# Performance work log

Hardware: AMD Instinct MI355X
Metric: run time of the kernel (lower is better)

Reference implementation:

```python
import jax, jax.numpy as jnp
import numpy as np

B, C, T, V = 8, 64, 16, 207
H, WSZ = 8, 4
EPS = 1e-5


def setup_inputs() -> dict:
    key = jax.random.key(0)
    ks = jax.random.split(key, 16)
    def w(k, shape):
        return jax.random.normal(k, shape, jnp.float32) * 0.02
    inp = {"x": jax.random.normal(ks[0], (B, C, T, V), jnp.float32)}
    for i, s in enumerate("ab"):
        o = 1 + i * 4
        inp[f"qkv_w_{s}"] = w(ks[o], (C, 3 * C))
        inp[f"qkv_b_{s}"] = jnp.zeros((3 * C,), jnp.float32)
        inp[f"proj_w_{s}"] = w(ks[o + 1], (C, C))
        inp[f"proj_b_{s}"] = jnp.zeros((C,), jnp.float32)
        inp[f"ffn_w1_{s}"] = w(ks[o + 2], (C, 4 * C))
        inp[f"ffn_b1_{s}"] = jnp.zeros((4 * C,), jnp.float32)
        inp[f"ffn_w2_{s}"] = w(ks[o + 3], (4 * C, C))
        inp[f"ffn_b2_{s}"] = jnp.zeros((C,), jnp.float32)
        inp[f"ln_{s}1_g"] = jnp.ones((C, T, V), jnp.float32)
        inp[f"ln_{s}1_b"] = jnp.zeros((C, T, V), jnp.float32)
        inp[f"ln_{s}2_g"] = jnp.ones((C, T, V), jnp.float32)
        inp[f"ln_{s}2_b"] = jnp.zeros((C, T, V), jnp.float32)
    inp["n_head"] = H
    inp["window_size"] = WSZ
    return inp


def _layer_norm(x, g, b):
    # LayerNorm over (C, T, V) dims of [B, C, T, V]
    mu = jnp.mean(x, axis=(1, 2, 3), keepdims=True)
    var = jnp.var(x, axis=(1, 2, 3), keepdims=True)
    return (x - mu) / jnp.sqrt(var + EPS) * g + b


def _window_att(x, wqkv, bqkv, wo, bo, n_head, wsz):
    # Joint spatio-temporal attention within windows of `wsz` timesteps.
    b_, c_, t_, v_ = x.shape
    nw = t_ // wsz
    dh = c_ // n_head
    # [B,C,T,V] -> [B,T,V,C] -> [B,nW, wsz*V, C]
    xt = jnp.transpose(x, (0, 2, 3, 1)).reshape(b_, nw, wsz * v_, c_)
    qkv = xt @ wqkv + bqkv  # [B,nW,N,3C]
    q, k, v = jnp.split(qkv, 3, axis=-1)
    def heads(t):
        return t.reshape(b_, nw, -1, n_head, dh).transpose(0, 1, 3, 2, 4)  # [B,nW,H,N,dh]
    q, k, v = heads(q), heads(k), heads(v)
    scale = 1.0 / jnp.sqrt(jnp.asarray(dh, jnp.float32))
    att = jax.nn.softmax(jnp.einsum('bwhnd,bwhmd->bwhnm', q, k) * scale, axis=-1)
    out = jnp.einsum('bwhnm,bwhmd->bwhnd', att, v)
    out = out.transpose(0, 1, 3, 2, 4).reshape(b_, nw, wsz * v_, c_) @ wo + bo
    return out.reshape(b_, t_, v_, c_).transpose(0, 3, 1, 2)


def _ffn(x, w1, b1, w2, b2):
    h = jax.nn.relu(jnp.einsum('bctv,cd->bdtv', x, w1) + b1[None, :, None, None])
    return jnp.einsum('bdtv,dc->bctv', h, w2) + b2[None, :, None, None]


def _block(x, wqkv, bqkv, wo, bo, w1, b1, w2, b2, g1, be1, g2, be2, n_head, wsz):
    x = _window_att(x, wqkv, bqkv, wo, bo, n_head, wsz) + x
    x = _layer_norm(x, g1, be1)
    x = _ffn(x, w1, b1, w2, b2) + x
    x = _layer_norm(x, g2, be2)
    # cyclic shift along time by shift_pixel = wsz // 2
    return jnp.roll(x, -(wsz // 2), axis=2)


def reference(x, qkv_w_a, qkv_b_a, proj_w_a, proj_b_a, ffn_w1_a, ffn_b1_a, ffn_w2_a, ffn_b2_a,
              ln_a1_g, ln_a1_b, ln_a2_g, ln_a2_b,
              qkv_w_b, qkv_b_b, proj_w_b, proj_b_b, ffn_w1_b, ffn_b1_b, ffn_w2_b, ffn_b2_b,
              ln_b1_g, ln_b1_b, ln_b2_g, ln_b2_b, n_head, window_size):
    x = _block(x, qkv_w_a, qkv_b_a, proj_w_a, proj_b_a, ffn_w1_a, ffn_b1_a, ffn_w2_a, ffn_b2_a,
               ln_a1_g, ln_a1_b, ln_a2_g, ln_a2_b, n_head, window_size)
    x = _block(x, qkv_w_b, qkv_b_b, proj_w_b, proj_b_b, ffn_w1_b, ffn_b1_b, ffn_w2_b, ffn_b2_b,
               ln_b1_g, ln_b1_b, ln_b2_g, ln_b2_b, n_head, window_size)
    return x
```

## Files before the change

### kernel.cpp

```cpp
#include <hip/hip_runtime.h>
#include <hip/hip_bf16.h>

#define Bb  8
#define Cc  64
#define Tt  16
#define Vv  207
#define Hh  8
#define DH  8
#define NW  4
#define WSZ 4
#define Nn  (WSZ*Vv)
#define NP  832
#define TV  (Tt*Vv)
#define CTV (Cc*Tt*Vv)
#define S   (Bb*CTV)
#define NBWH (Bb*NW*Hh)
#define EPSF 1e-5f
#define QSCALE 0.51006971401146f

typedef __attribute__((ext_vector_type(4))) short bf16x4;
typedef __attribute__((ext_vector_type(4))) float f32x4;
typedef __attribute__((ext_vector_type(2))) unsigned int u32x2;

static __device__ __forceinline__ short f2bf(float f) {
    union { float f; unsigned u; } v; v.f = f;
    unsigned r = (v.u + 0x7FFFu + ((v.u >> 16) & 1u)) >> 16;
    return (short)r;
}

static __device__ __forceinline__ bf16x4 pack4(float a, float b, float c, float d) {
    unsigned ua = __builtin_bit_cast(unsigned, a) + 0x8000u;
    unsigned ub = __builtin_bit_cast(unsigned, b) + 0x8000u;
    unsigned uc = __builtin_bit_cast(unsigned, c) + 0x8000u;
    unsigned ud = __builtin_bit_cast(unsigned, d) + 0x8000u;
    u32x2 t;
    t[0] = (ua >> 16) | (ub & 0xFFFF0000u);
    t[1] = (uc >> 16) | (ud & 0xFFFF0000u);
    return __builtin_bit_cast(bf16x4, t);
}

__global__ void prep_kernel(short* __restrict__ qb, short* __restrict__ kb,
                            short* __restrict__ vtb, float* __restrict__ stats) {
    int i = blockIdx.x*256 + threadIdx.x;
    if (i < 64) stats[i] = 0.f;
    if (i < NBWH*NP*8) {
        int bwh = i / (NP*8); int rest = i % (NP*8);
        int n = rest >> 3; int d = 8 + (rest & 7);
        kb[((size_t)bwh*NP + n)*16 + d] = 0;
        int d2 = 8 + rest / NP; int n2 = rest % NP;
        vtb[((size_t)bwh*16 + d2)*NP + n2] = (d2 == 8) ? (short)0x3F80 : (short)0;
    }
    if (i < NBWH*32) {
        int bwh = i >> 5; int rest = i & 31;
        int n = Nn + (rest >> 3); int d = rest & 7;
        qb[((size_t)bwh*NP + n)*8 + d] = 0;
        kb[((size_t)bwh*NP + n)*16 + d] = 0;
        int d3 = rest >> 2; int n3 = Nn + (rest & 3);
        vtb[((size_t)bwh*16 + d3)*NP + n3] = 0;
    }
}

__global__ __launch_bounds__(256) void qkv_kernel(const float* __restrict__ src,
        const float* __restrict__ st, const float* __restrict__ g, const float* __restrict__ be,
        const float* __restrict__ w, const float* __restrict__ bias,
        short* __restrict__ qb, short* __restrict__ kb, short* __restrict__ vtb) {
    __shared__ short wqs[3072*4];
    __shared__ float bqs[192];
    __shared__ short os[64*196];
    int tid = threadIdx.x;
    int b = blockIdx.x / 52;
    int r0 = (blockIdx.x % 52) * 64;
    const float* xb = src + (size_t)b*CTV;
    for (int s = tid; s < 3072; s += 256) {
        int nt = s >> 8; int kc = (s >> 6) & 3; int ln = s & 63;
        int li = ln & 15; int q = ln >> 4;
        bf16x4 f;
        #pragma unroll
        for (int j = 0; j < 4; ++j)
            f[j] = f2bf(w[(kc*16 + q*4 + j)*192 + nt*16 + li]);
        *((bf16x4*)&wqs[s*4]) = f;
    }
    if (tid < 192) bqs[tid] = bias[tid];
    __syncthreads();

    int lane = tid & 63; int wv = tid >> 6;
    int l15 = lane & 15; int quad = lane >> 4;
    int r = r0 + wv*16 + l15;
    int rc = (r < TV) ? r : TV-1;
    int t = rc / Vv; int vv = rc - t*Vv;
    float mean = 0.f, rstd = 0.f; int off;
    if (st) {
        mean = st[b*2] * (1.0f/CTV);
        float var = st[b*2+1] * (1.0f/CTV) - mean*mean;
        rstd = rsqrtf(var + EPSF);
        off = ((t+2)&15)*Vv + vv;
    } else off = rc;

    bf16x4 xf[4];
    #pragma unroll
    for (int kc = 0; kc < 4; ++kc) {
        #pragma unroll
        for (int j = 0; j < 4; ++j) {
            int idx = (kc*16 + quad*4 + j)*TV + off;
            float xv = xb[idx];
            if (st) xv = (xv - mean)*rstd*g[idx] + be[idx];
            xf[kc][j] = f2bf(xv);
        }
    }

    f32x4 accv[12];
    #pragma unroll
    for (int nt = 0; nt < 12; ++nt) {
        float4 bb = *((const float4*)&bqs[nt*16 + quad*4]);
        f32x4 acc = {bb.x, bb.y, bb.z, bb.w};
        #pragma unroll
        for (int kc = 0; kc < 4; ++kc) {
            bf16x4 wf = *((const bf16x4*)&wqs[((nt*4 + kc)*64 + lane)*4]);
            acc = __builtin_amdgcn_mfma_f32_16x16x16bf16_1k(wf, xf[kc], acc, 0, 0, 0);
        }
        accv[nt] = acc;
    }

    int pos = wv*16 + l15;
    #pragma unroll
    for (int nt = 0; nt < 12; ++nt) {
        f32x4 a = accv[nt];
        bf16x4 pk = (nt < 4) ? pack4(a[0]*QSCALE, a[1]*QSCALE, a[2]*QSCALE, a[3]*QSCALE)
                             : pack4(a[0], a[1], a[2], a[3]);
        *((bf16x4*)&os[pos*196 + nt*16 + quad*4]) = pk;
    }
    __syncthreads();

    int pp = tid & 63;
    int rr = r0 + pp;
    bool pv = rr < TV;
    int rrc = pv ? rr : TV-1;
    int t4 = rrc / Vv; int vv4 = rrc - t4*Vv;
    int n2 = (t4 & 3)*Vv + vv4;
    int wbase = (b*NW + (t4 >> 2))*Hh;
    #pragma unroll
    for (int i = 0; i < 2; ++i) {
        int h = i*4 + wv;
        if (pv) {
            bf16x4 q0 = *((const bf16x4*)&os[pp*196 + h*8]);
            bf16x4 q1 = *((const bf16x4*)&os[pp*196 + h*8 + 4]);
            short* qd = &qb[((size_t)(wbase + h)*NP + n2)*8];
            *((bf16x4*)qd) = q0; *((bf16x4*)(qd+4)) = q1;
            bf16x4 k0 = *((const bf16x4*)&os[pp*196 + 64 + h*8]);
            bf16x4 k1 = *((const bf16x4*)&os[pp*196 + 64 + h*8 + 4]);
            short* kd = &kb[((size_t)(wbase + h)*NP + n2)*16];
            *((bf16x4*)kd) = k0; *((bf16x4*)(kd+4)) = k1;
        }
    }
    #pragma unroll
    for (int i = 0; i < 16; ++i) {
        int hd = i*4 + wv;
        if (pv)
            vtb[((size_t)(wbase + (hd >> 3))*16 + (hd & 7))*NP + n2] = os[pp*196 + 128 + hd];
    }
}

__global__ __launch_bounds__(1024) void attn_kernel(const short* __restrict__ qb,
        const short* __restrict__ kb, const short* __restrict__ vtb,
        short* __restrict__ att) {
    __shared__ short ks[NP*20];
    __shared__ short vs[10*840];
    int bwh = blockIdx.x;
    int tid = threadIdx.x;
    int lane = tid & 63;
    int wv = tid >> 6;
    int quad = lane >> 4;
    int l15 = lane & 15;

    const u32x2* kg = (const u32x2*)(kb + (size_t)bwh*NP*16);
    for (int idx = tid; idx < NP*4; idx += 1024) {
        int n = idx >> 2; int j = idx & 3;
        *((u32x2*)&ks[n*20 + j*4]) = kg[idx];
    }
    const u32x2* vg = (const u32x2*)(vtb + (size_t)bwh*16*NP);
    for (int idx = tid; idx < 9*208; idx += 1024) {
        int rr = idx / 208; int j = idx % 208;
        *((u32x2*)&vs[rr*840 + j*4]) = vg[rr*208 + j];
    }
    if (tid < 210) *((u32x2*)&vs[9*840 + tid*4]) = (u32x2){0u, 0u};
    __syncthreads();

    int nm = (wv < 4) ? 4 : 3;
    const short* qbase = qb + (size_t)bwh*NP*8;
    bf16x4 aq[4];
    f32x4 oacc[4];
    #pragma unroll
    for (int i = 0; i < 4; ++i) {
        aq[i] = (bf16x4){0,0,0,0};
        oacc[i] = (f32x4){0.f,0.f,0.f,0.f};
        if (i < nm && quad < 2)
            aq[i] = *(const bf16x4*)(qbase + (((wv + 16*i)*16 + l15)*8 + quad*4));
    }
    const short* kls = &ks[l15*20 + quad*4];
    const short* vls = &vs[((l15 < 9) ? l15 : 9)*840 + quad*4];

    for (int nt = 0; nt < 52; ++nt) {
        bf16x4 ak = *(const bf16x4*)(kls + nt*320);
        bf16x4 av = *(const bf16x4*)(vls + nt*16);
        bool mask = (nt == 51) && (quad == 3);
        #pragma unroll
        for (int i = 0; i < 4; ++i) {
            if (i < nm) {
                f32x4 s = __builtin_amdgcn_mfma_f32_16x16x16bf16_1k(
                              ak, aq[i], (f32x4){0.f,0.f,0.f,0.f}, 0, 0, 0);
                bf16x4 pb = pack4(__builtin_amdgcn_exp2f(s[0]), __builtin_amdgcn_exp2f(s[1]),
                                  __builtin_amdgcn_exp2f(s[2]), __builtin_amdgcn_exp2f(s[3]));
                if (mask) pb = (bf16x4){0,0,0,0};
                oacc[i] = __builtin_amdgcn_mfma_f32_16x16x16bf16_1k(av, pb, oacc[i], 0, 0, 0);
            }
        }
    }
    int h = bwh & 7; int bw = bwh >> 3;
    #pragma unroll
    for (int i = 0; i < 4; ++i) {
        if (i < nm) {
            float ls = __shfl(oacc[i][0], 32 + l15, 64);
            float inv = 1.f / ls;
            int m = (wv + 16*i)*16 + l15;
            if (quad < 2 && m < Nn) {
                bf16x4 ov = pack4(oacc[i][0]*inv, oacc[i][1]*inv,
                                  oacc[i][2]*inv, oacc[i][3]*inv);
                *((bf16x4*)&att[((size_t)bw*Nn + m)*Cc + h*DH + quad*4]) = ov;
            }
        }
    }
}

__global__ __launch_bounds__(256) void proj_kernel(const short* __restrict__ att,
        const float* __restrict__ wo, const float* __restrict__ bo,
        const float* __restrict__ resid,
        const float* __restrict__ st, const float* __restrict__ g, const float* __restrict__ be,
        float* __restrict__ out, float* __restrict__ stats) {
    __shared__ short wos[1024*4];
    __shared__ float bos[64];
    __shared__ float r1[256], r2[256];
    int tid = threadIdx.x;
    int b = blockIdx.x / 52;
    int r0 = (blockIdx.x % 52) * 64;
    const float* xb = resid + (size_t)b*CTV;
    for (int s = tid; s < 1024; s += 256) {
        int nt = s >> 8; int kc = (s >> 6) & 3; int ln = s & 63;
        int li = ln & 15; int q = ln >> 4;
        bf16x4 f;
        #pragma unroll
        for (int j = 0; j < 4; ++j)
            f[j] = f2bf(wo[(kc*16 + q*4 + j)*64 + nt*16 + li]);
        *((bf16x4*)&wos[s*4]) = f;
    }
    if (tid < 64) bos[tid] = bo[tid];
    __syncthreads();

    int lane = tid & 63; int wv = tid >> 6;
    int l15 = lane & 15; int quad = lane >> 4;
    int r = r0 + wv*16 + l15;
    bool valid = r < TV;
    int rc = valid ? r : TV-1;
    int t = rc / Vv; int vv = rc - t*Vv;
    int n = (t & 3)*Vv + vv;
    int bw = b*NW + (t >> 2);
    const short* arow = att + ((size_t)bw*Nn + n)*Cc;
    bf16x4 af[4];
    #pragma unroll
    for (int kc = 0; kc < 4; ++kc)
        af[kc] = *((const bf16x4*)&arow[kc*16 + quad*4]);

    f32x4 acc[4];
    #pragma unroll
    for (int nt = 0; nt < 4; ++nt) {
        float4 bb = *((const float4*)&bos[nt*16 + quad*4]);
        acc[nt] = (f32x4){bb.x, bb.y, bb.z, bb.w};
        #pragma unroll
        for (int kc = 0; kc < 4; ++kc) {
            bf16x4 wf = *((const bf16x4*)&wos[((nt*4 + kc)*64 + lane)*4]);
            acc[nt] = __builtin_amdgcn_mfma_f32_16x16x16bf16_1k(wf, af[kc], acc[nt], 0, 0, 0);
        }
    }
    float mean = 0.f, rstd = 0.f; int off;
    if (st) {
        mean = st[b*2] * (1.0f/CTV);
        float var = st[b*2+1] * (1.0f/CTV) - mean*mean;
        rstd = rsqrtf(var + EPSF);
        off = ((t+2)&15)*Vv + vv;
    } else off = rc;
    float s1 = 0.f, s2 = 0.f;
    if (valid) {
        #pragma unroll
        for (int nt = 0; nt < 4; ++nt) {
            #pragma unroll
            for (int j = 0; j < 4; ++j) {
                int c_out = nt*16 + quad*4 + j;
                int ridx = c_out*TV + off;
                float xv = xb[ridx];
                if (st) xv = (xv - mean)*rstd*g[ridx] + be[ridx];
                float val = acc[nt][j] + xv;
                out[(size_t)b*CTV + (size_t)c_out*TV + r] = val;
                s1 += val; s2 += val*val;
            }
        }
    }
    r1[tid] = s1; r2[tid] = s2;
    __syncthreads();
    for (int o = 128; o > 0; o >>= 1) {
        if (tid < o) { r1[tid] += r1[tid+o]; r2[tid] += r2[tid+o]; }
        __syncthreads();
    }
    if (tid == 0) { atomicAdd(&stats[b*2], r1[0]); atomicAdd(&stats[b*2+1], r2[0]); }
}

__global__ void ln_apply_kernel(const float* __restrict__ x,
                                const float* __restrict__ g,
                                const float* __restrict__ be,
                                const float* __restrict__ stats,
                                float* __restrict__ out,
                                int shift) {
    int idx = blockIdx.x*256 + threadIdx.x;
    if (idx >= S) return;
    int b = idx / CTV; int r = idx % CTV;
    int c = r / TV; int q2 = r % TV; int t = q2 / Vv; int vv = q2 % Vv;
    float mean = stats[b*2] * (1.0f/CTV);
    float var  = stats[b*2+1] * (1.0f/CTV) - mean*mean;
    float rstd = rsqrtf(var + EPSF);
    float val = (x[idx]-mean)*rstd*g[r] + be[r];
    int tout = (t - shift + Tt) % Tt;
    size_t oidx = ((size_t)(b*Cc + c)*Tt + tout)*Vv + vv;
    out[oidx] = val;
}

__global__ __launch_bounds__(256) void ffn_kernel(const float* __restrict__ xin,
        const float* __restrict__ st, const float* __restrict__ g, const float* __restrict__ be,
        const float* __restrict__ w1, const float* __restrict__ b1,
        const float* __restrict__ w2, const float* __restrict__ b2,
        float* __restrict__ out, float* __restrict__ stats) {
    __shared__ short w1s[4096*4];
    __shared__ short w2s[4096*4];
    __shared__ short xsf[1024*4];
    __shared__ float b1s[256];
    __shared__ float b2s[64];
    __shared__ float r1s[256], r2s[256];
    int tid = threadIdx.x;
    int b = blockIdx.x / 52;
    int r0 = (blockIdx.x % 52) * 64;
    const float* xb = xin + (size_t)b*CTV;
    float mean = st[b*2] * (1.0f/CTV);
    float var  = st[b*2+1] * (1.0f/CTV) - mean*mean;
    float rstd = rsqrtf(var + EPSF);

    for (int s2 = tid; s2 < 4096; s2 += 256) {
        int nt = s2 >> 8; int kc = (s2 >> 6) & 3; int ln = s2 & 63;
        int l15 = ln & 15; int quad = ln >> 4;
        bf16x4 f;
        #pragma unroll
        for (int j = 0; j < 4; ++j)
            f[j] = f2bf(w1[(kc*16 + quad*4 + j)*256 + nt*16 + l15]);
        *((bf16x4*)&w1s[s2*4]) = f;
    }
    for (int s2 = tid; s2 < 4096; s2 += 256) {
        int nt = s2 >> 8; int ct = (s2 >> 6) & 3; int ln = s2 & 63;
        int l15 = ln & 15; int quad = ln >> 4;
        bf16x4 f;
        #pragma unroll
        for (int j = 0; j < 4; ++j)
            f[j] = f2bf(w2[(nt*16 + quad*4 + j)*64 + ct*16 + l15]);
        *((bf16x4*)&w2s[s2*4]) = f;
    }
    for (int s2 = tid; s2 < 1024; s2 += 256) {
        int wv2 = s2 >> 8; int kc = (s2 >> 6) & 3; int ln = s2 & 63;
        int l15 = ln & 15; int quad = ln >> 4;
        int r = r0 + wv2*16 + l15; if (r >= TV) r = TV-1;
        bf16x4 f;
        #pragma unroll
        for (int j = 0; j < 4; ++j) {
            int idx = (kc*16 + quad*4 + j)*TV + r;
            f[j] = f2bf((xb[idx] - mean)*rstd*g[idx] + be[idx]);
        }
        *((bf16x4*)&xsf[s2*4]) = f;
    }
    b1s[tid] = b1[tid];
    if (tid < 64) b2s[tid] = b2[tid];
    __syncthreads();

    int lane = tid & 63; int wv = tid >> 6;
    int l15 = lane & 15; int quad = lane >> 4;
    bf16x4 xf[4];
    #pragma unroll
    for (int kc = 0; kc < 4; ++kc)
        xf[kc] = *((const bf16x4*)&xsf[((wv*4 + kc)*64 + lane)*4]);

    f32x4 oacc[4];
    #pragma unroll
    for (int ct = 0; ct < 4; ++ct) oacc[ct] = (f32x4){0.f,0.f,0.f,0.f};

    for (int nt = 0; nt < 16; ++nt) {
        float4 bb = *((const float4*)&b1s[nt*16 + quad*4]);
        f32x4 acc = {bb.x, bb.y, bb.z, bb.w};
        #pragma unroll
        for (int kc = 0; kc < 4; ++kc) {
            bf16x4 wf = *((const bf16x4*)&w1s[((nt*4 + kc)*64 + lane)*4]);
            acc = __builtin_amdgcn_mfma_f32_16x16x16bf16_1k(wf, xf[kc], acc, 0, 0, 0);
        }
        bf16x4 pf = pack4(fmaxf(acc[0], 0.f), fmaxf(acc[1], 0.f),
                          fmaxf(acc[2], 0.f), fmaxf(acc[3], 0.f));
        #pragma unroll
        for (int ct = 0; ct < 4; ++ct) {
            bf16x4 wf2 = *((const bf16x4*)&w2s[((nt*4 + ct)*64 + lane)*4]);
            oacc[ct] = __builtin_amdgcn_mfma_f32_16x16x16bf16_1k(wf2, pf, oacc[ct], 0, 0, 0);
        }
    }
    int r = r0 + wv*16 + l15;
    float s1 = 0.f, s2 = 0.f;
    if (r < TV) {
        #pragma unroll
        for (int ct = 0; ct < 4; ++ct) {
            #pragma unroll
            for (int j = 0; j < 4; ++j) {
                int c_out = ct*16 + quad*4 + j;
                int idx = c_out*TV + r;
                float xv = (xb[idx] - mean)*rstd*g[idx] + be[idx];
                float val = oacc[ct][j] + b2s[c_out] + xv;
                out[(size_t)b*CTV + idx] = val;
                s1 += val; s2 += val*val;
            }
        }
    }
    r1s[tid] = s1; r2s[tid] = s2;
    __syncthreads();
    for (int o = 128; o > 0; o >>= 1) {
        if (tid < o) { r1s[tid] += r1s[tid+o]; r2s[tid] += r2s[tid+o]; }
        __syncthreads();
    }
    if (tid == 0) { atomicAdd(&stats[b*2], r1s[0]); atomicAdd(&stats[b*2+1], r2s[0]); }
}

extern "C" void kernel_launch(void* const* d_in, const int* in_sizes, int n_in,
                              void* d_out, int out_size, void* d_ws, size_t ws_size,
                              hipStream_t stream) {
    const float* xin = (const float*)d_in[0];

    float* bufA  = (float*)d_ws;
    float* bufB  = bufA + S;
    float* stats = bufB + S;
    short* qb    = (short*)(stats + 64);
    short* kb    = qb + (size_t)NBWH*NP*8;
    short* vtb   = kb + (size_t)NBWH*NP*16;
    short* att   = vtb + (size_t)NBWH*16*NP;

    const float* A0  = (const float*)d_in[1+0*12];
    const float* A1  = (const float*)d_in[1+0*12+1];
    const float* A2  = (const float*)d_in[1+0*12+2];
    const float* A3  = (const float*)d_in[1+0*12+3];
    const float* A4  = (const float*)d_in[1+0*12+4];
    const float* A5  = (const float*)d_in[1+0*12+5];
    const float* A6  = (const float*)d_in[1+0*12+6];
    const float* A7  = (const float*)d_in[1+0*12+7];
    const float* A8  = (const float*)d_in[1+0*12+8];
    const float* A9  = (const float*)d_in[1+0*12+9];
    const float* A10 = (const float*)d_in[1+0*12+10];
    const float* A11 = (const float*)d_in[1+0*12+11];
    const float* B0  = (const float*)d_in[1+1*12];
    const float* B1  = (const float*)d_in[1+1*12+1];
    const float* B2  = (const float*)d_in[1+1*12+2];
    const float* B3  = (const float*)d_in[1+1*12+3];
    const float* B4  = (const float*)d_in[1+1*12+4];
    const float* B5  = (const float*)d_in[1+1*12+5];
    const float* B6  = (const float*)d_in[1+1*12+6];
    const float* B7  = (const float*)d_in[1+1*12+7];
    const float* B8  = (const float*)d_in[1+1*12+8];
    const float* B9  = (const float*)d_in[1+1*12+9];
    const float* B10 = (const float*)d_in[1+1*12+10];
    const float* B11 = (const float*)d_in[1+1*12+11];

    float* st1a = stats + 0;
    float* st2a = stats + 16;
    float* st1b = stats + 32;
    float* st2b = stats + 48;

    prep_kernel<<<(NBWH*NP*8 + 255)/256, 256, 0, stream>>>(qb, kb, vtb, stats);

    qkv_kernel<<<Bb*52, 256, 0, stream>>>(xin, nullptr, nullptr, nullptr, A0, A1, qb, kb, vtb);
    attn_kernel<<<NBWH, 1024, 0, stream>>>(qb, kb, vtb, att);
    proj_kernel<<<Bb*52, 256, 0, stream>>>(att, A2, A3, xin, nullptr, nullptr, nullptr, bufB, st1a);
    ffn_kernel<<<Bb*52, 256, 0, stream>>>(bufB, st1a, A8, A9, A4, A5, A6, A7, bufB, st2a);
    qkv_kernel<<<Bb*52, 256, 0, stream>>>(bufB, st2a, A10, A11, B0, B1, qb, kb, vtb);
    attn_kernel<<<NBWH, 1024, 0, stream>>>(qb, kb, vtb, att);
    proj_kernel<<<Bb*52, 256, 0, stream>>>(att, B2, B3, bufB, st2a, A10, A11, bufA, st1b);
    ffn_kernel<<<Bb*52, 256, 0, stream>>>(bufA, st1b, B8, B9, B4, B5, B6, B7, bufA, st2b);
    ln_apply_kernel<<<(S+255)/256, 256, 0, stream>>>(bufA, B10, B11, st2b, (float*)d_out, WSZ/2);
}
```

Baseline: 304.3 us.

## Pre-pack bf16 MFMA weight fragments once and store Q/K/V in fragment layout

A new prep kernel converts all four weight matrices of both layers into bf16 MFMA fragment order once per call, so the qkv, proj and ffn blocks only copy packed fragments into LDS instead of each re-gathering and converting fp32 weights. The qkv kernel now writes Q, K and V straight into per-tile MFMA fragment layout, which lets the attention kernel load K/V with plain contiguous copies and index LDS by lane without padding. Padding and ones-column setup moves to a separate pads kernel. This adds an extra launch and scattered 2-byte V stores in qkv in exchange for cheaper weight staging in hundreds of blocks and simpler attention loads.

```diff
diff --git a/kernel.cpp b/kernel.cpp
--- a/kernel.cpp
+++ b/kernel.cpp
@@ -17,6 +17,8 @@
 #define NBWH (Bb*NW*Hh)
 #define EPSF 1e-5f
 #define QSCALE 0.51006971401146f
+#define FRAG_BWH (52*64*4)
+#define LAYER_WSZ 49152
 
 typedef __attribute__((ext_vector_type(4))) short bf16x4;
 typedef __attribute__((ext_vector_type(4))) float f32x4;
@@ -39,46 +41,76 @@
     return __builtin_bit_cast(bf16x4, t);
 }
 
-__global__ void prep_kernel(short* __restrict__ qb, short* __restrict__ kb,
-                            short* __restrict__ vtb, float* __restrict__ stats) {
+__global__ void prep_w_kernel(const float* __restrict__ qa, const float* __restrict__ pa,
+                              const float* __restrict__ w1a, const float* __restrict__ w2a,
+                              const float* __restrict__ qbw, const float* __restrict__ pbw,
+                              const float* __restrict__ w1b, const float* __restrict__ w2b,
+                              short* __restrict__ wf, float* __restrict__ stats) {
+    if (blockIdx.x == 0 && threadIdx.x < 64) stats[threadIdx.x] = 0.f;
     int i = blockIdx.x*256 + threadIdx.x;
-    if (i < 64) stats[i] = 0.f;
-    if (i < NBWH*NP*8) {
-        int bwh = i / (NP*8); int rest = i % (NP*8);
-        int n = rest >> 3; int d = 8 + (rest & 7);
-        kb[((size_t)bwh*NP + n)*16 + d] = 0;
-        int d2 = 8 + rest / NP; int n2 = rest % NP;
-        vtb[((size_t)bwh*16 + d2)*NP + n2] = (d2 == 8) ? (short)0x3F80 : (short)0;
-    }
-    if (i < NBWH*32) {
-        int bwh = i >> 5; int rest = i & 31;
-        int n = Nn + (rest >> 3); int d = rest & 7;
-        qb[((size_t)bwh*NP + n)*8 + d] = 0;
-        kb[((size_t)bwh*NP + n)*16 + d] = 0;
-        int d3 = rest >> 2; int n3 = Nn + (rest & 3);
-        vtb[((size_t)bwh*16 + d3)*NP + n3] = 0;
-    }
+    int l = i / 12288; int f = i % 12288;
+    const float* qw = l ? qbw : qa;
+    const float* pw = l ? pbw : pa;
+    const float* w1 = l ? w1b : w1a;
+    const float* w2 = l ? w2b : w2a;
+    short* dst = wf + l*LAYER_WSZ;
+    bf16x4 out;
+    if (f < 3072) {
+        int s = f; int nt = s>>8; int kc = (s>>6)&3; int ln = s&63;
+        int li = ln&15; int q = ln>>4;
+        #pragma unroll
+        for (int j = 0; j < 4; ++j) out[j] = f2bf(qw[(kc*16+q*4+j)*192 + nt*16+li]);
+        *((bf16x4*)&dst[s*4]) = out;
+    } else if (f < 4096) {
+        int s = f-3072; int nt = s>>8; int kc = (s>>6)&3; int ln = s&63;
+        int li = ln&15; int q = ln>>4;
+        #pragma unroll
+        for (int j = 0; j < 4; ++j) out[j] = f2bf(pw[(kc*16+q*4+j)*64 + nt*16+li]);
+        *((bf16x4*)&dst[12288 + s*4]) = out;
+    } else if (f < 8192) {
+        int s = f-4096; int nt = s>>8; int kc = (s>>6)&3; int ln = s&63;
+        int li = ln&15; int q = ln>>4;
+        #pragma unroll
+        for (int j = 0; j < 4; ++j) out[j] = f2bf(w1[(kc*16+q*4+j)*256 + nt*16+li]);
+        *((bf16x4*)&dst[16384 + s*4]) = out;
+    } else {
+        int s = f-8192; int nt = s>>8; int ct = (s>>6)&3; int ln = s&63;
+        int li = ln&15; int q = ln>>4;
+        #pragma unroll
+        for (int j = 0; j < 4; ++j) out[j] = f2bf(w2[(nt*16+q*4+j)*64 + ct*16+li]);
+        *((bf16x4*)&dst[32768 + s*4]) = out;
+    }
+}
+
+__global__ void prep_pads_kernel(short* __restrict__ qf, short* __restrict__ kf,
+                                 short* __restrict__ vf) {
+    int i = blockIdx.x*256 + threadIdx.x;
+    int bwh = i / 1664; int rest = i % 1664;
+    int nt = rest >> 5; int u = rest & 31;
+    size_t base = (size_t)bwh*FRAG_BWH + nt*256;
+    *((u32x2*)&qf[base + (32+u)*4]) = (u32x2){0u,0u};
+    *((u32x2*)&kf[base + (32+u)*4]) = (u32x2){0u,0u};
+    int vlane = (u>>3)*16 + 8 + (u&7);
+    short v = ((u&7) == 0) ? (short)0x3F80 : (short)0;
+    bf16x4 vv4 = {v,v,v,v};
+    *((bf16x4*)&vf[base + vlane*4]) = vv4;
 }
 
 __global__ __launch_bounds__(256) void qkv_kernel(const float* __restrict__ src,
         const float* __restrict__ st, const float* __restrict__ g, const float* __restrict__ be,
-        const float* __restrict__ w, const float* __restrict__ bias,
-        short* __restrict__ qb, short* __restrict__ kb, short* __restrict__ vtb) {
-    __shared__ short wqs[3072*4];
+        const short* __restrict__ wfq, const float* __restrict__ bias,
+        short* __restrict__ qf, short* __restrict__ kf, short* __restrict__ vf) {
+    __shared__ short wqs[12288];
     __shared__ float bqs[192];
     __shared__ short os[64*196];
     int tid = threadIdx.x;
     int b = blockIdx.x / 52;
     int r0 = (blockIdx.x % 52) * 64;
     const float* xb = src + (size_t)b*CTV;
-    for (int s = tid; s < 3072; s += 256) {
-        int nt = s >> 8; int kc = (s >> 6) & 3; int ln = s & 63;
-        int li = ln & 15; int q = ln >> 4;
-        bf16x4 f;
-        #pragma unroll
-        for (int j = 0; j < 4; ++j)
-            f[j] = f2bf(w[(kc*16 + q*4 + j)*192 + nt*16 + li]);
-        *((bf16x4*)&wqs[s*4]) = f;
+    {
+        const u32x2* wsrc = (const u32x2*)wfq;
+        u32x2* wdst = (u32x2*)wqs;
+        for (int s = tid; s < 3072; s += 256) wdst[s] = wsrc[s];
     }
     if (tid < 192) bqs[tid] = bias[tid];
     __syncthreads();
@@ -115,8 +147,8 @@
         f32x4 acc = {bb.x, bb.y, bb.z, bb.w};
         #pragma unroll
         for (int kc = 0; kc < 4; ++kc) {
-            bf16x4 wf = *((const bf16x4*)&wqs[((nt*4 + kc)*64 + lane)*4]);
-            acc = __builtin_amdgcn_mfma_f32_16x16x16bf16_1k(wf, xf[kc], acc, 0, 0, 0);
+            bf16x4 wf2 = *((const bf16x4*)&wqs[((nt*4 + kc)*64 + lane)*4]);
+            acc = __builtin_amdgcn_mfma_f32_16x16x16bf16_1k(wf2, xf[kc], acc, 0, 0, 0);
         }
         accv[nt] = acc;
     }
@@ -137,34 +169,38 @@
     int rrc = pv ? rr : TV-1;
     int t4 = rrc / Vv; int vv4 = rrc - t4*Vv;
     int n2 = (t4 & 3)*Vv + vv4;
+    int nt2 = n2 >> 4; int l15n = n2 & 15;
+    int quadn = (n2 & 15) >> 2; int jn = n2 & 3;
     int wbase = (b*NW + (t4 >> 2))*Hh;
-    #pragma unroll
-    for (int i = 0; i < 2; ++i) {
-        int h = i*4 + wv;
-        if (pv) {
+    if (pv) {
+        #pragma unroll
+        for (int i = 0; i < 2; ++i) {
+            int h = i*4 + wv;
+            size_t fb = ((size_t)(wbase+h)*52 + nt2)*256;
             bf16x4 q0 = *((const bf16x4*)&os[pp*196 + h*8]);
             bf16x4 q1 = *((const bf16x4*)&os[pp*196 + h*8 + 4]);
-            short* qd = &qb[((size_t)(wbase + h)*NP + n2)*8];
-            *((bf16x4*)qd) = q0; *((bf16x4*)(qd+4)) = q1;
+            *((bf16x4*)&qf[fb + l15n*4])        = q0;
+            *((bf16x4*)&qf[fb + (16 + l15n)*4]) = q1;
             bf16x4 k0 = *((const bf16x4*)&os[pp*196 + 64 + h*8]);
             bf16x4 k1 = *((const bf16x4*)&os[pp*196 + 64 + h*8 + 4]);
-            short* kd = &kb[((size_t)(wbase + h)*NP + n2)*16];
-            *((bf16x4*)kd) = k0; *((bf16x4*)(kd+4)) = k1;
-        }
-    }
-    #pragma unroll
-    for (int i = 0; i < 16; ++i) {
-        int hd = i*4 + wv;
-        if (pv)
-            vtb[((size_t)(wbase + (hd >> 3))*16 + (hd & 7))*NP + n2] = os[pp*196 + 128 + hd];
-    }
-}
-
-__global__ __launch_bounds__(1024) void attn_kernel(const short* __restrict__ qb,
-        const short* __restrict__ kb, const short* __restrict__ vtb,
+            *((bf16x4*)&kf[fb + l15n*4])        = k0;
+            *((bf16x4*)&kf[fb + (16 + l15n)*4]) = k1;
+        }
+        #pragma unroll
+        for (int i = 0; i < 16; ++i) {
+            int hd = i*4 + wv;
+            int h = hd >> 3; int d = hd & 7;
+            vf[(((size_t)(wbase+h)*52 + nt2)*64 + quadn*16 + d)*4 + jn]
+                = os[pp*196 + 128 + hd];
+        }
+    }
+}
+
+__global__ __launch_bounds__(1024) void attn_kernel(const short* __restrict__ qf,
+        const short* __restrict__ kf, const short* __restrict__ vf,
         short* __restrict__ att) {
-    __shared__ short ks[NP*20];
-    __shared__ short vs[10*840];
+    __shared__ short ks2[FRAG_BWH];
+    __shared__ short vs2[FRAG_BWH];
     int bwh = blockIdx.x;
     int tid = threadIdx.x;
     int lane = tid & 63;
@@ -172,36 +208,29 @@
     int quad = lane >> 4;
     int l15 = lane & 15;
 
-    const u32x2* kg = (const u32x2*)(kb + (size_t)bwh*NP*16);
-    for (int idx = tid; idx < NP*4; idx += 1024) {
-        int n = idx >> 2; int j = idx & 3;
-        *((u32x2*)&ks[n*20 + j*4]) = kg[idx];
-    }
-    const u32x2* vg = (const u32x2*)(vtb + (size_t)bwh*16*NP);
-    for (int idx = tid; idx < 9*208; idx += 1024) {
-        int rr = idx / 208; int j = idx % 208;
-        *((u32x2*)&vs[rr*840 + j*4]) = vg[rr*208 + j];
-    }
-    if (tid < 210) *((u32x2*)&vs[9*840 + tid*4]) = (u32x2){0u, 0u};
+    {
+        const u32x2* kg = (const u32x2*)(kf + (size_t)bwh*FRAG_BWH);
+        const u32x2* vg = (const u32x2*)(vf + (size_t)bwh*FRAG_BWH);
+        u32x2* kd = (u32x2*)ks2; u32x2* vd = (u32x2*)vs2;
+        for (int idx = tid; idx < 3328; idx += 1024) { kd[idx] = kg[idx]; vd[idx] = vg[idx]; }
+    }
     __syncthreads();
 
     int nm = (wv < 4) ? 4 : 3;
-    const short* qbase = qb + (size_t)bwh*NP*8;
+    const short* qbase = qf + (size_t)bwh*FRAG_BWH;
     bf16x4 aq[4];
     f32x4 oacc[4];
     #pragma unroll
     for (int i = 0; i < 4; ++i) {
         aq[i] = (bf16x4){0,0,0,0};
         oacc[i] = (f32x4){0.f,0.f,0.f,0.f};
-        if (i < nm && quad < 2)
-            aq[i] = *(const bf16x4*)(qbase + (((wv + 16*i)*16 + l15)*8 + quad*4));
-    }
-    const short* kls = &ks[l15*20 + quad*4];
-    const short* vls = &vs[((l15 < 9) ? l15 : 9)*840 + quad*4];
+        if (i < nm)
+            aq[i] = *(const bf16x4*)(qbase + ((wv + 16*i)*256 + lane*4));
+    }
 
     for (int nt = 0; nt < 52; ++nt) {
-        bf16x4 ak = *(const bf16x4*)(kls + nt*320);
-        bf16x4 av = *(const bf16x4*)(vls + nt*16);
+        bf16x4 ak = *(const bf16x4*)&ks2[nt*256 + lane*4];
+        bf16x4 av = *(const bf16x4*)&vs2[nt*256 + lane*4];
         bool mask = (nt == 51) && (quad == 3);
         #pragma unroll
         for (int i = 0; i < 4; ++i) {
@@ -232,25 +261,21 @@
 }
 
 __global__ __launch_bounds__(256) void proj_kernel(const short* __restrict__ att,
-        const float* __restrict__ wo, const float* __restrict__ bo,
+        const short* __restrict__ wfp, const float* __restrict__ bo,
         const float* __restrict__ resid,
         const float* __restrict__ st, const float* __restrict__ g, const float* __restrict__ be,
         float* __restrict__ out, float* __restrict__ stats) {
-    __shared__ short wos[1024*4];
+    __shared__ short wos[4096];
     __shared__ float bos[64];
     __shared__ float r1[256], r2[256];
     int tid = threadIdx.x;
     int b = blockIdx.x / 52;
     int r0 = (blockIdx.x % 52) * 64;
     const float* xb = resid + (size_t)b*CTV;
-    for (int s = tid; s < 1024; s += 256) {
-        int nt = s >> 8; int kc = (s >> 6) & 3; int ln = s & 63;
-        int li = ln & 15; int q = ln >> 4;
-        bf16x4 f;
-        #pragma unroll
-        for (int j = 0; j < 4; ++j)
-            f[j] = f2bf(wo[(kc*16 + q*4 + j)*64 + nt*16 + li]);
-        *((bf16x4*)&wos[s*4]) = f;
+    {
+        const u32x2* wsrc = (const u32x2*)wfp;
+        u32x2* wdst = (u32x2*)wos;
+        for (int s = tid; s < 1024; s += 256) wdst[s] = wsrc[s];
     }
     if (tid < 64) bos[tid] = bo[tid];
     __syncthreads();
@@ -276,8 +301,8 @@
         acc[nt] = (f32x4){bb.x, bb.y, bb.z, bb.w};
         #pragma unroll
         for (int kc = 0; kc < 4; ++kc) {
-            bf16x4 wf = *((const bf16x4*)&wos[((nt*4 + kc)*64 + lane)*4]);
-            acc[nt] = __builtin_amdgcn_mfma_f32_16x16x16bf16_1k(wf, af[kc], acc[nt], 0, 0, 0);
+            bf16x4 wf2 = *((const bf16x4*)&wos[((nt*4 + kc)*64 + lane)*4]);
+            acc[nt] = __builtin_amdgcn_mfma_f32_16x16x16bf16_1k(wf2, af[kc], acc[nt], 0, 0, 0);
         }
     }
     float mean = 0.f, rstd = 0.f; int off;
@@ -333,12 +358,12 @@
 
 __global__ __launch_bounds__(256) void ffn_kernel(const float* __restrict__ xin,
         const float* __restrict__ st, const float* __restrict__ g, const float* __restrict__ be,
-        const float* __restrict__ w1, const float* __restrict__ b1,
-        const float* __restrict__ w2, const float* __restrict__ b2,
+        const short* __restrict__ wf1, const float* __restrict__ b1,
+        const short* __restrict__ wf2g, const float* __restrict__ b2,
         float* __restrict__ out, float* __restrict__ stats) {
-    __shared__ short w1s[4096*4];
-    __shared__ short w2s[4096*4];
-    __shared__ short xsf[1024*4];
+    __shared__ short w1s[16384];
+    __shared__ short w2s[16384];
+    __shared__ short xsf[4096];
     __shared__ float b1s[256];
     __shared__ float b2s[64];
     __shared__ float r1s[256], r2s[256];
@@ -350,23 +375,11 @@
     float var  = st[b*2+1] * (1.0f/CTV) - mean*mean;
     float rstd = rsqrtf(var + EPSF);
 
-    for (int s2 = tid; s2 < 4096; s2 += 256) {
-        int nt = s2 >> 8; int kc = (s2 >> 6) & 3; int ln = s2 & 63;
-        int l15 = ln & 15; int quad = ln >> 4;
-        bf16x4 f;
-        #pragma unroll
-        for (int j = 0; j < 4; ++j)
-            f[j] = f2bf(w1[(kc*16 + quad*4 + j)*256 + nt*16 + l15]);
-        *((bf16x4*)&w1s[s2*4]) = f;
-    }
-    for (int s2 = tid; s2 < 4096; s2 += 256) {
-        int nt = s2 >> 8; int ct = (s2 >> 6) & 3; int ln = s2 & 63;
-        int l15 = ln & 15; int quad = ln >> 4;
-        bf16x4 f;
-        #pragma unroll
-        for (int j = 0; j < 4; ++j)
-            f[j] = f2bf(w2[(nt*16 + quad*4 + j)*64 + ct*16 + l15]);
-        *((bf16x4*)&w2s[s2*4]) = f;
+    {
+        const u32x2* s1p = (const u32x2*)wf1;
+        const u32x2* s2p = (const u32x2*)wf2g;
+        u32x2* d1 = (u32x2*)w1s; u32x2* d2 = (u32x2*)w2s;
+        for (int s = tid; s < 4096; s += 256) { d1[s] = s1p[s]; d2[s] = s2p[s]; }
     }
     for (int s2 = tid; s2 < 1024; s2 += 256) {
         int wv2 = s2 >> 8; int kc = (s2 >> 6) & 3; int ln = s2 & 63;
@@ -400,15 +413,15 @@
         f32x4 acc = {bb.x, bb.y, bb.z, bb.w};
         #pragma unroll
         for (int kc = 0; kc < 4; ++kc) {
-            bf16x4 wf = *((const bf16x4*)&w1s[((nt*4 + kc)*64 + lane)*4]);
-            acc = __builtin_amdgcn_mfma_f32_16x16x16bf16_1k(wf, xf[kc], acc, 0, 0, 0);
+            bf16x4 wfv = *((const bf16x4*)&w1s[((nt*4 + kc)*64 + lane)*4]);
+            acc = __builtin_amdgcn_mfma_f32_16x16x16bf16_1k(wfv, xf[kc], acc, 0, 0, 0);
         }
         bf16x4 pf = pack4(fmaxf(acc[0], 0.f), fmaxf(acc[1], 0.f),
                           fmaxf(acc[2], 0.f), fmaxf(acc[3], 0.f));
         #pragma unroll
         for (int ct = 0; ct < 4; ++ct) {
-            bf16x4 wf2 = *((const bf16x4*)&w2s[((nt*4 + ct)*64 + lane)*4]);
-            oacc[ct] = __builtin_amdgcn_mfma_f32_16x16x16bf16_1k(wf2, pf, oacc[ct], 0, 0, 0);
+            bf16x4 wfv2 = *((const bf16x4*)&w2s[((nt*4 + ct)*64 + lane)*4]);
+            oacc[ct] = __builtin_amdgcn_mfma_f32_16x16x16bf16_1k(wfv2, pf, oacc[ct], 0, 0, 0);
         }
     }
     int r = r0 + wv*16 + l15;
@@ -444,50 +457,61 @@
     float* bufA  = (float*)d_ws;
     float* bufB  = bufA + S;
     float* stats = bufB + S;
-    short* qb    = (short*)(stats + 64);
-    short* kb    = qb + (size_t)NBWH*NP*8;
-    short* vtb   = kb + (size_t)NBWH*NP*16;
-    short* att   = vtb + (size_t)NBWH*16*NP;
-
-    const float* A0  = (const float*)d_in[1+0*12];
-    const float* A1  = (const float*)d_in[1+0*12+1];
-    const float* A2  = (const float*)d_in[1+0*12+2];
-    const float* A3  = (const float*)d_in[1+0*12+3];
-    const float* A4  = (const float*)d_in[1+0*12+4];
-    const float* A5  = (const float*)d_in[1+0*12+5];
-    const float* A6  = (const float*)d_in[1+0*12+6];
-    const float* A7  = (const float*)d_in[1+0*12+7];
-    const float* A8  = (const float*)d_in[1+0*12+8];
-    const float* A9  = (const float*)d_in[1+0*12+9];
-    const float* A10 = (const float*)d_in[1+0*12+10];
-    const float* A11 = (const float*)d_in[1+0*12+11];
-    const float* B0  = (const float*)d_in[1+1*12];
-    const float* B1  = (const float*)d_in[1+1*12+1];
-    const float* B2  = (const float*)d_in[1+1*12+2];
-    const float* B3  = (const float*)d_in[1+1*12+3];
-    const float* B4  = (const float*)d_in[1+1*12+4];
-    const float* B5  = (const float*)d_in[1+1*12+5];
-    const float* B6  = (const float*)d_in[1+1*12+6];
-    const float* B7  = (const float*)d_in[1+1*12+7];
-    const float* B8  = (const float*)d_in[1+1*12+8];
-    const float* B9  = (const float*)d_in[1+1*12+9];
-    const float* B10 = (const float*)d_in[1+1*12+10];
-    const float* B11 = (const float*)d_in[1+1*12+11];
+    short* qf    = (short*)(stats + 64);
+    short* kf    = qf + (size_t)NBWH*FRAG_BWH;
+    short* vf    = kf + (size_t)NBWH*FRAG_BWH;
+    short* att   = vf + (size_t)NBWH*FRAG_BWH;
+    short* wf    = att + (size_t)32*Nn*64;
+
+    const float* A0  = (const float*)d_in[1];
+    const float* A1  = (const float*)d_in[2];
+    const float* A2  = (const float*)d_in[3];
+    const float* A3  = (const float*)d_in[4];
+    const float* A4  = (const float*)d_in[5];
+    const float* A5  = (const float*)d_in[6];
+    const float* A6  = (const float*)d_in[7];
+    const float* A7  = (const float*)d_in[8];
+    const float* A8  = (const float*)d_in[9];
+    const float* A9  = (const float*)d_in[10];
+    const float* A10 = (const float*)d_in[11];
+    const float* A11 = (const float*)d_in[12];
+    const float* B0  = (const float*)d_in[13];
+    const float* B1  = (const float*)d_in[14];
+    const float* B2  = (const float*)d_in[15];
+    const float* B3  = (const float*)d_in[16];
+    const float* B4  = (const float*)d_in[17];
+    const float* B5  = (const float*)d_in[18];
+    const float* B6  = (const float*)d_in[19];
+    const float* B7  = (const float*)d_in[20];
+    const float* B8  = (const float*)d_in[21];
+    const float* B9  = (const float*)d_in[22];
+    const float* B10 = (const float*)d_in[23];
+    const float* B11 = (const float*)d_in[24];
 
     float* st1a = stats + 0;
     float* st2a = stats + 16;
     float* st1b = stats + 32;
     float* st2b = stats + 48;
 
-    prep_kernel<<<(NBWH*NP*8 + 255)/256, 256, 0, stream>>>(qb, kb, vtb, stats);
-
-    qkv_kernel<<<Bb*52, 256, 0, stream>>>(xin, nullptr, nullptr, nullptr, A0, A1, qb, kb, vtb);
-    attn_kernel<<<NBWH, 1024, 0, stream>>>(qb, kb, vtb, att);
-    proj_kernel<<<Bb*52, 256, 0, stream>>>(att, A2, A3, xin, nullptr, nullptr, nullptr, bufB, st1a);
-    ffn_kernel<<<Bb*52, 256, 0, stream>>>(bufB, st1a, A8, A9, A4, A5, A6, A7, bufB, st2a);
-    qkv_kernel<<<Bb*52, 256, 0, stream>>>(bufB, st2a, A10, A11, B0, B1, qb, kb, vtb);
-    attn_kernel<<<NBWH, 1024, 0, stream>>>(qb, kb, vtb, att);
-    proj_kernel<<<Bb*52, 256, 0, stream>>>(att, B2, B3, bufB, st2a, A10, A11, bufA, st1b);
-    ffn_kernel<<<Bb*52, 256, 0, stream>>>(bufA, st1b, B8, B9, B4, B5, B6, B7, bufA, st2b);
+    short* wfA = wf;
+    short* wfB = wf + LAYER_WSZ;
+
+    prep_w_kernel<<<96, 256, 0, stream>>>(A0, A2, A4, A6, B0, B2, B4, B6, wf, stats);
+    prep_pads_kernel<<<1664, 256, 0, stream>>>(qf, kf, vf);
+
+    qkv_kernel<<<Bb*52, 256, 0, stream>>>(xin, nullptr, nullptr, nullptr,
+                                          wfA, A1, qf, kf, vf);
+    attn_kernel<<<NBWH, 1024, 0, stream>>>(qf, kf, vf, att);
+    proj_kernel<<<Bb*52, 256, 0, stream>>>(att, wfA + 12288, A3, xin,
+                                           nullptr, nullptr, nullptr, bufB, st1a);
+    ffn_kernel<<<Bb*52, 256, 0, stream>>>(bufB, st1a, A8, A9,
+                                          wfA + 16384, A5, wfA + 32768, A7, bufB, st2a);
+    qkv_kernel<<<Bb*52, 256, 0, stream>>>(bufB, st2a, A10, A11,
+                                          wfB, B1, qf, kf, vf);
+    attn_kernel<<<NBWH, 1024, 0, stream>>>(qf, kf, vf, att);
+    proj_kernel<<<Bb*52, 256, 0, stream>>>(att, wfB + 12288, B3, bufB,
+                                           st2a, A10, A11, bufA, st1b);
+    ffn_kernel<<<Bb*52, 256, 0, stream>>>(bufA, st1b, B8, B9,
+                                          wfB + 16384, B5, wfB + 32768, B7, bufA, st2b);
     ln_apply_kernel<<<(S+255)/256, 256, 0, stream>>>(bufA, B10, B11, st2b, (float*)d_out, WSZ/2);
 }
```

New measurement: 301.6 us. About the same (-0.9%).
